# Optimization experiments

Hardware: AMD Instinct MI355X
Metric: run time of the kernel (lower is better)

Reference implementation:

```python
import jax, jax.numpy as jnp
import numpy as np

N_NODES = 200000
IN_DIM = 128
HID = 64
WALK_LEN = 16          # max_step + 1
NUM_WALKS = 16         # = hidden_graphs, walks per graph
N_GRAPHS = 1024
PEN = 32
N_CLASSES = 10
BN_EPS = 1e-5


def setup_inputs() -> dict:
    key = jax.random.key(0)
    ks = jax.random.split(key, 16)
    x = jax.random.normal(ks[0], (N_NODES, IN_DIM), dtype=jnp.float32)
    walks = jax.random.randint(ks[1], (N_GRAPHS * NUM_WALKS, WALK_LEN), 0, N_NODES)
    # each graph contributes NUM_WALKS consecutive walks
    walk_batch = jnp.repeat(jnp.arange(N_GRAPHS), NUM_WALKS)
    s = 1.0 / np.sqrt(HID)
    return {
        "x": x,
        "walks": walks,
        "walk_batch": walk_batch,
        "W_enc": jax.random.normal(ks[2], (HID, IN_DIM), jnp.float32) / np.sqrt(IN_DIM),
        "b_enc": jnp.zeros((HID,), jnp.float32),
        "W_ih": jax.random.uniform(ks[3], (3 * HID, HID), jnp.float32, -s, s),
        "W_hh": jax.random.uniform(ks[4], (3 * HID, HID), jnp.float32, -s, s),
        "b_ih": jax.random.uniform(ks[5], (3 * HID,), jnp.float32, -s, s),
        "b_hh": jax.random.uniform(ks[6], (3 * HID,), jnp.float32, -s, s),
        "gamma": jnp.ones((HID,), jnp.float32),
        "beta": jnp.zeros((HID,), jnp.float32),
        "W1": jax.random.normal(ks[7], (PEN, HID), jnp.float32) / np.sqrt(HID),
        "b1": jnp.zeros((PEN,), jnp.float32),
        "W2": jax.random.normal(ks[8], (N_CLASSES, PEN), jnp.float32) / np.sqrt(PEN),
        "b2": jnp.zeros((N_CLASSES,), jnp.float32),
    }


def _gru_cell(h, xt, W_ih, W_hh, b_ih, b_hh):
    # PyTorch GRU gate math
    gi = xt @ W_ih.T + b_ih            # [W, 3H]
    gh = h @ W_hh.T + b_hh             # [W, 3H]
    i_r, i_z, i_n = jnp.split(gi, 3, axis=-1)
    h_r, h_z, h_n = jnp.split(gh, 3, axis=-1)
    r = jax.nn.sigmoid(i_r + h_r)
    z = jax.nn.sigmoid(i_z + h_z)
    n = jnp.tanh(i_n + r * h_n)
    return (1.0 - z) * n + z * h


def reference(x, walks, walk_batch, W_enc, b_enc, W_ih, W_hh, b_ih, b_hh,
              gamma, beta, W1, b1, W2, b2):
    # feature encoder on all nodes, then gather along walks
    x_enc = x @ W_enc.T + b_enc                     # [N, H]
    walk_feats = x_enc[walks]                       # [W, L, H] gather
    xs = jnp.swapaxes(walk_feats, 0, 1)             # [L, W, H]

    def step(h, xt):
        return _gru_cell(h, xt, W_ih, W_hh, b_ih, b_hh), None

    h0 = jnp.zeros((walks.shape[0], HID), walk_feats.dtype)
    h_final, _ = jax.lax.scan(step, h0, xs)         # [W, H] last hidden state

    # segment-mean pooling per graph
    seg_sum = jax.ops.segment_sum(h_final, walk_batch, num_segments=N_GRAPHS)
    cnt = jax.ops.segment_sum(jnp.ones((walks.shape[0],), h_final.dtype),
                              walk_batch, num_segments=N_GRAPHS)
    graph_enc = seg_sum / jnp.maximum(cnt, 1.0)[:, None]   # [B, H]

    # BatchNorm1d (training mode: batch statistics, biased variance)
    mean = jnp.mean(graph_enc, axis=0)
    var = jnp.mean(jnp.square(graph_enc - mean), axis=0)
    gn = (graph_enc - mean) / jnp.sqrt(var + BN_EPS) * gamma + beta

    h1 = jax.nn.relu(gn @ W1.T + b1)                # dropout p=0 -> identity
    logits = h1 @ W2.T + b2
    return jax.nn.log_softmax(logits, axis=1)
```

## Files before the change

### kernel.cpp

```cpp
#include <hip/hip_runtime.h>
#include <stdint.h>

typedef _Float16 half8 __attribute__((ext_vector_type(8)));
typedef _Float16 half4 __attribute__((ext_vector_type(4)));
typedef float f32x4 __attribute__((ext_vector_type(4)));

#define MFMA_F16(A, B, C) __builtin_amdgcn_mfma_f32_16x16x32_f16(A, B, C, 0, 0, 0)

#define NN 200000
#define NT 3125
#define GSTRIDE 512

__device__ __forceinline__ half8 cvt8(const float* p) {
  half8 a;
#pragma unroll
  for (int e = 0; e < 8; ++e) a[e] = (_Float16)p[e];
  return a;
}

__device__ __forceinline__ void gload_lds16(const void* gp, void* lp) {
  __builtin_amdgcn_global_load_lds(
      (const __attribute__((address_space(1))) uint32_t*)(gp),
      (__attribute__((address_space(3))) uint32_t*)(lp), 16, 0, 0);
}

__global__ __launch_bounds__(256, 2) void k_enc(const float* __restrict__ x,
                                                const float* __restrict__ Wenc,
                                                const float* __restrict__ benc,
                                                _Float16* __restrict__ xenc) {
  __shared__ float xl[2][64 * 128];
  __shared__ _Float16 wlds[16 * 64 * 8];

  const int tid = threadIdx.x;
  const int lane = tid & 63, wv = tid >> 6;
  const int r = lane & 15, g = lane >> 4;

  const int t0 = blockIdx.x;
#pragma unroll
  for (int i = 0; i < 8; ++i) {
    int row = wv * 16 + 2 * i + (lane >> 5);
    int grow = t0 * 64 + row;
    if (grow >= NN) grow = NN - 1;
    int scol = ((lane & 31) * 16) ^ ((row & 7) << 4);
    gload_lds16((const char*)(x + (size_t)grow * 128) + scol,
                (char*)&xl[0][0] + (wv * 16 + 2 * i) * 512);
  }

  for (int i4 = tid; i4 < 2048; i4 += 256) {
    int idx = i4 * 4;
    f32x4 v = *(const f32x4*)(Wenc + idx);
    int j = idx >> 7, k = idx & 127;
    int tile = (j >> 4) * 4 + (k >> 5);
    int ln = ((k >> 3) & 3) * 16 + (j & 15);
    half4 h;
    h[0] = (_Float16)v[0]; h[1] = (_Float16)v[1];
    h[2] = (_Float16)v[2]; h[3] = (_Float16)v[3];
    *(half4*)&wlds[(tile * 64 + ln) * 8 + (k & 7)] = h;
  }
  __syncthreads();

  half8 W[4][4];
#pragma unroll
  for (int jt = 0; jt < 4; ++jt)
#pragma unroll
    for (int kt = 0; kt < 4; ++kt)
      W[jt][kt] = *(const half8*)&wlds[((jt * 4 + kt) * 64 + lane) * 8];

  float bb[4][4];
#pragma unroll
  for (int jt = 0; jt < 4; ++jt)
#pragma unroll
    for (int rr = 0; rr < 4; ++rr) bb[jt][rr] = benc[jt * 16 + g * 4 + rr];

  const int sw = (r & 7) << 4;
  int buf = 0;

  for (int t = t0; t < NT; t += GSTRIDE) {
    int tn = t + GSTRIDE;
    if (tn < NT) {
#pragma unroll
      for (int i = 0; i < 8; ++i) {
        int row = wv * 16 + 2 * i + (lane >> 5);
        int grow = tn * 64 + row;
        if (grow >= NN) grow = NN - 1;
        int scol = ((lane & 31) * 16) ^ ((row & 7) << 4);
        gload_lds16((const char*)(x + (size_t)grow * 128) + scol,
                    (char*)&xl[buf ^ 1][0] + (wv * 16 + 2 * i) * 512);
      }
      asm volatile("s_waitcnt vmcnt(8)" ::: "memory");
    } else {
      asm volatile("s_waitcnt vmcnt(0)" ::: "memory");
    }
    __builtin_amdgcn_sched_barrier(0);

    const char* rp = (const char*)&xl[buf][0] + (wv * 16 + r) * 512;
    f32x4 acc[4];
#pragma unroll
    for (int jt = 0; jt < 4; ++jt)
      acc[jt] = (f32x4){bb[jt][0], bb[jt][1], bb[jt][2], bb[jt][3]};

#pragma unroll
    for (int kt = 0; kt < 4; ++kt) {
      f32x4 v0 = *(const f32x4*)(rp + ((kt * 128 + g * 32) ^ sw));
      f32x4 v1 = *(const f32x4*)(rp + ((kt * 128 + g * 32 + 16) ^ sw));
      half8 a;
#pragma unroll
      for (int e = 0; e < 4; ++e) {
        a[e] = (_Float16)v0[e];
        a[4 + e] = (_Float16)v1[e];
      }
#pragma unroll
      for (int jt = 0; jt < 4; ++jt)
        acc[jt] = MFMA_F16(W[jt][kt], a, acc[jt]);
    }

    int node = t * 64 + wv * 16 + r;
    if (node < NN) {
#pragma unroll
      for (int jt = 0; jt < 4; ++jt) {
        half4 o;
        o[0] = (_Float16)acc[jt][0]; o[1] = (_Float16)acc[jt][1];
        o[2] = (_Float16)acc[jt][2]; o[3] = (_Float16)acc[jt][3];
        *(half4*)&xenc[(size_t)node * 64 + jt * 16 + g * 4] = o;
      }
    }
    buf ^= 1;
  }
}

__global__ __launch_bounds__(256, 1) void k_gru(const _Float16* __restrict__ xenc,
                                                const int* __restrict__ walks,
                                                const float* __restrict__ Wih,
                                                const float* __restrict__ Whh,
                                                const float* __restrict__ bih,
                                                const float* __restrict__ bhh,
                                                float* __restrict__ genc) {
  __shared__ _Float16 wih_lds[24 * 64 * 8];
  __shared__ _Float16 whh_lds[24 * 64 * 8];
  __shared__ _Float16 h_lds[4][16 * 64];
  __shared__ int ids[4][256];

  const int tid = threadIdx.x;
  const int lane = tid & 63, wv = tid >> 6;
  const int r = lane & 15, g = lane >> 4;

  for (int idx = tid; idx < 192 * 64; idx += 256) {
    int j = idx >> 6, k = idx & 63;
    int tile = (j >> 4) * 2 + (k >> 5);
    int ln = ((k >> 3) & 3) * 16 + (j & 15);
    int off = (tile * 64 + ln) * 8 + (k & 7);
    wih_lds[off] = (_Float16)Wih[idx];
    whh_lds[off] = (_Float16)Whh[idx];
  }

  const int gph = blockIdx.x * 4 + wv;
  {
    const int* wp = walks + gph * 256;
    int4 v = *(const int4*)(wp + lane * 4);
    int vals[4] = {v.x, v.y, v.z, v.w};
#pragma unroll
    for (int i = 0; i < 4; ++i) {
      int m = lane * 4 + i;
      ids[wv][(m & 15) * 16 + (m >> 4)] = vals[i];
    }
  }
  for (int i = lane; i < 16 * 64; i += 64) h_lds[wv][i] = (_Float16)0.f;

  __syncthreads();

  half8 Bih[12][2], Bhh[12][2];
#pragma unroll
  for (int jt = 0; jt < 12; ++jt)
#pragma unroll
    for (int kt = 0; kt < 2; ++kt) {
      Bih[jt][kt] = *(const half8*)&wih_lds[((jt * 2 + kt) * 64 + lane) * 8];
      Bhh[jt][kt] = *(const half8*)&whh_lds[((jt * 2 + kt) * 64 + lane) * 8];
    }

  float brz[8], bin4[4], bhn4[4];
#pragma unroll
  for (int jt = 0; jt < 8; ++jt) brz[jt] = bih[jt * 16 + r] + bhh[jt * 16 + r];
#pragma unroll
  for (int jt = 0; jt < 4; ++jt) {
    bin4[jt] = bih[128 + jt * 16 + r];
    bhn4[jt] = bhh[128 + jt * 16 + r];
  }

  f32x4 h[4];
#pragma unroll
  for (int jt = 0; jt < 4; ++jt) h[jt] = (f32x4){0.f, 0.f, 0.f, 0.f};

  char* hbase = (char*)&h_lds[wv][0];
  const int swz = (r & 7) << 4;

  half8 AxA0, AxA1, AxB0, AxB1;
  {
    int n0 = ids[wv][0 * 16 + r];
    const _Float16* p0 = xenc + (size_t)n0 * 64 + g * 8;
    AxA0 = *(const half8*)p0;
    AxA1 = *(const half8*)(p0 + 32);
    int n1 = ids[wv][1 * 16 + r];
    const _Float16* p1 = xenc + (size_t)n1 * 64 + g * 8;
    AxB0 = *(const half8*)p1;
    AxB1 = *(const half8*)(p1 + 32);
  }

#define GRU_STEP(T, AX0, AX1)                                                  \
  {                                                                            \
    half8 Ah0 = *(const half8*)(hbase + ((r * 128 + g * 16) ^ swz));           \
    half8 Ah1 = *(const half8*)(hbase + ((r * 128 + 64 + g * 16) ^ swz));      \
    f32x4 aRZ[8], aIN[4], aHN[4];                                              \
    _Pragma("unroll") for (int jt = 0; jt < 8; ++jt)                           \
        aRZ[jt] = (f32x4){brz[jt], brz[jt], brz[jt], brz[jt]};                 \
    _Pragma("unroll") for (int jt = 0; jt < 4; ++jt) {                         \
      aIN[jt] = (f32x4){bin4[jt], bin4[jt], bin4[jt], bin4[jt]};               \
      aHN[jt] = (f32x4){bhn4[jt], bhn4[jt], bhn4[jt], bhn4[jt]};               \
    }                                                                          \
    _Pragma("unroll") for (int jt = 0; jt < 8; ++jt) {                         \
      aRZ[jt] = MFMA_F16(AX0, Bih[jt][0], aRZ[jt]);                            \
      aRZ[jt] = MFMA_F16(AX1, Bih[jt][1], aRZ[jt]);                            \
    }                                                                          \
    _Pragma("unroll") for (int jt = 0; jt < 4; ++jt) {                         \
      aIN[jt] = MFMA_F16(AX0, Bih[8 + jt][0], aIN[jt]);                        \
      aIN[jt] = MFMA_F16(AX1, Bih[8 + jt][1], aIN[jt]);                        \
    }                                                                          \
                            \
    {                                                                          \
      int nid = ids[wv][(((T) + 2) & 15) * 16 + r];                            \
      const _Float16* xp = xenc + (size_t)nid * 64 + g * 8;                    \
      AX0 = *(const half8*)xp;                                                 \
      AX1 = *(const half8*)(xp + 32);                                          \
    }                                                                          \
    _Pragma("unroll") for (int jt = 0; jt < 8; ++jt) {                         \
      aRZ[jt] = MFMA_F16(Ah0, Bhh[jt][0], aRZ[jt]);                            \
      aRZ[jt] = MFMA_F16(Ah1, Bhh[jt][1], aRZ[jt]);                            \
    }                                                                          \
    _Pragma("unroll") for (int jt = 0; jt < 4; ++jt) {                         \
      aHN[jt] = MFMA_F16(Ah0, Bhh[8 + jt][0], aHN[jt]);                        \
      aHN[jt] = MFMA_F16(Ah1, Bhh[8 + jt][1], aHN[jt]);                        \
    }                                                                          \
    _Pragma("unroll") for (int jt = 0; jt < 4; ++jt)                           \
        _Pragma("unroll") for (int rr = 0; rr < 4; ++rr) {                     \
      float pr = aRZ[jt][rr];                                                  \
      float pz = aRZ[4 + jt][rr];                                              \
      float rg = __builtin_amdgcn_rcpf(1.f + __expf(-pr));                     \
      float zg = __builtin_amdgcn_rcpf(1.f + __expf(-pz));                     \
      float pn = aIN[jt][rr] + rg * aHN[jt][rr];                               \
      float e2 = __expf(2.f * pn);                                             \
      float nn = 1.f - 2.f * __builtin_amdgcn_rcpf(e2 + 1.f);                  \
      h[jt][rr] = (1.f - zg) * nn + zg * h[jt][rr];                            \
    }                                                                          \
    if ((T) < 15) {                                                            \
      _Pragma("unroll") for (int jt = 0; jt < 4; ++jt)                         \
          _Pragma("unroll") for (int rr = 0; rr < 4; ++rr) {                   \
        int row = g * 4 + rr;                                                  \
        int byte = (row * 128 + (jt * 16 + r) * 2) ^ ((row & 7) << 4);         \
        *(_Float16*)(hbase + byte) = (_Float16)h[jt][rr];                      \
      }                                                                        \
    }                                                                          \
  }

  for (int t = 0; t < 16; t += 2) {
    GRU_STEP(t, AxA0, AxA1);
    GRU_STEP(t + 1, AxB0, AxB1);
  }
#undef GRU_STEP

#pragma unroll
  for (int jt = 0; jt < 4; ++jt) {
    float s = h[jt][0] + h[jt][1] + h[jt][2] + h[jt][3];
    s += __shfl_xor(s, 16);
    s += __shfl_xor(s, 32);
    if (g == 0) genc[gph * 64 + jt * 16 + r] = s * 0.0625f;
  }
}

__global__ __launch_bounds__(1024) void k_stats(const float* __restrict__ genc,
                                                const float* __restrict__ gamma,
                                                const float* __restrict__ beta,
                                                float* __restrict__ ss) {
  __shared__ float sum_s[16][64], sq_s[16][64];
  int j = threadIdx.x & 63, grp = threadIdx.x >> 6;
  float s = 0.f, q = 0.f;
#pragma unroll 4
  for (int rr = 0; rr < 64; ++rr) {
    float v = genc[(grp * 64 + rr) * 64 + j];
    s += v;
    q += v * v;
  }
  sum_s[grp][j] = s;
  sq_s[grp][j] = q;
  __syncthreads();
  if (grp == 0) {
    float S = 0.f, Q = 0.f;
#pragma unroll
    for (int k = 0; k < 16; ++k) {
      S += sum_s[k][j];
      Q += sq_s[k][j];
    }
    float mean = S * (1.f / 1024.f);
    float var = Q * (1.f / 1024.f) - mean * mean;
    float rstd = rsqrtf(var + 1e-5f);
    float sc = gamma[j] * rstd;
    ss[j] = sc;
    ss[64 + j] = beta[j] - mean * sc;
  }
}

__global__ __launch_bounds__(256, 1) void k_mlp(const float* __restrict__ genc,
                                                const float* __restrict__ ss,
                                                const float* __restrict__ W1,
                                                const float* __restrict__ b1,
                                                const float* __restrict__ W2,
                                                const float* __restrict__ b2,
                                                float* __restrict__ out) {
  __shared__ float w1[32 * 64], w2[10 * 32], bb1[32], bb2[10], sc[64], sh[64];
  const int tid = threadIdx.x;
  for (int i = tid; i < 32 * 64; i += 256) w1[i] = W1[i];
  for (int i = tid; i < 10 * 32; i += 256) w2[i] = W2[i];
  if (tid < 32) bb1[tid] = b1[tid];
  if (tid >= 32 && tid < 42) bb2[tid - 32] = b2[tid - 32];
  if (tid >= 64 && tid < 128) sc[tid - 64] = ss[tid - 64];
  if (tid >= 128 && tid < 192) sh[tid - 128] = ss[64 + tid - 128];
  __syncthreads();

  const int row = blockIdx.x * 256 + tid;
  float gn[64];
  const f32x4* gp = (const f32x4*)(genc + row * 64);
#pragma unroll
  for (int jq = 0; jq < 16; ++jq) {
    f32x4 v = gp[jq];
#pragma unroll
    for (int e = 0; e < 4; ++e) gn[jq * 4 + e] = v[e] * sc[jq * 4 + e] + sh[jq * 4 + e];
  }

  float h1[32];
#pragma unroll
  for (int i = 0; i < 32; ++i) {
    float a = bb1[i];
#pragma unroll
    for (int j = 0; j < 64; ++j) a += w1[i * 64 + j] * gn[j];
    h1[i] = fmaxf(a, 0.f);
  }

  float lg[10];
  float mx = -1e30f;
#pragma unroll
  for (int c = 0; c < 10; ++c) {
    float a = bb2[c];
#pragma unroll
    for (int i = 0; i < 32; ++i) a += w2[c * 32 + i] * h1[i];
    lg[c] = a;
    mx = fmaxf(mx, a);
  }
  float se = 0.f;
#pragma unroll
  for (int c = 0; c < 10; ++c) se += __expf(lg[c] - mx);
  float lse = mx + __logf(se);
#pragma unroll
  for (int c = 0; c < 10; ++c) out[row * 10 + c] = lg[c] - lse;
}

extern "C" void kernel_launch(void* const* d_in, const int* in_sizes, int n_in,
                              void* d_out, int out_size, void* d_ws, size_t ws_size,
                              hipStream_t stream) {
  const float* x = (const float*)d_in[0];
  const int* walks = (const int*)d_in[1];
  const float* Wenc = (const float*)d_in[3];
  const float* benc = (const float*)d_in[4];
  const float* Wih = (const float*)d_in[5];
  const float* Whh = (const float*)d_in[6];
  const float* bih = (const float*)d_in[7];
  const float* bhh = (const float*)d_in[8];
  const float* gamma = (const float*)d_in[9];
  const float* beta = (const float*)d_in[10];
  const float* W1 = (const float*)d_in[11];
  const float* b1 = (const float*)d_in[12];
  const float* W2 = (const float*)d_in[13];
  const float* b2 = (const float*)d_in[14];
  float* out = (float*)d_out;

  char* ws = (char*)d_ws;
  _Float16* xenc = (_Float16*)ws;
  float* genc = (float*)(ws + 25600000);
  float* ss = (float*)(ws + 25600000 + 262144);

  k_enc<<<dim3(GSTRIDE), dim3(256), 0, stream>>>(x, Wenc, benc, xenc);
  k_gru<<<dim3(256), dim3(256), 0, stream>>>(xenc, walks, Wih, Whh, bih, bhh, genc);
  k_stats<<<dim3(1), dim3(1024), 0, stream>>>(genc, gamma, beta, ss);
  k_mlp<<<dim3(4), dim3(256), 0, stream>>>(genc, ss, W1, b1, W2, b2, out);
}
```

Before: 85.92 us.

## Split each graph's GRU hidden units across two waves with double-buffered h

Each graph's GRU recurrence is now handled by two wavefronts, each computing half of the hidden units, instead of one wave per graph. The grid doubles to 512 blocks with two graphs per block. The hidden state goes through a double-buffered LDS array, and a block-wide barrier after every step exchanges the halves. This halves per-wave MFMA and register work on the serial recurrence and raises occupancy (launch bounds 2), at the cost of 16 barriers per block and duplicated x gathers.

```diff
diff --git a/kernel.cpp b/kernel.cpp
--- a/kernel.cpp
+++ b/kernel.cpp
@@ -128,7 +128,7 @@
   }
 }
 
-__global__ __launch_bounds__(256, 1) void k_gru(const _Float16* __restrict__ xenc,
+__global__ __launch_bounds__(256, 2) void k_gru(const _Float16* __restrict__ xenc,
                                                 const int* __restrict__ walks,
                                                 const float* __restrict__ Wih,
                                                 const float* __restrict__ Whh,
@@ -137,12 +137,15 @@
                                                 float* __restrict__ genc) {
   __shared__ _Float16 wih_lds[24 * 64 * 8];
   __shared__ _Float16 whh_lds[24 * 64 * 8];
-  __shared__ _Float16 h_lds[4][16 * 64];
-  __shared__ int ids[4][256];
+  __shared__ _Float16 h_lds[2][2][16 * 64];
+  __shared__ int ids[2][256];
 
   const int tid = threadIdx.x;
   const int lane = tid & 63, wv = tid >> 6;
   const int r = lane & 15, g = lane >> 4;
+  const int p = wv & 1;
+  const int gl = wv >> 1;
+  const int gph = blockIdx.x * 2 + gl;
 
   for (int idx = tid; idx < 192 * 64; idx += 256) {
     int j = idx >> 6, k = idx & 63;
@@ -153,125 +156,132 @@
     whh_lds[off] = (_Float16)Whh[idx];
   }
 
-  const int gph = blockIdx.x * 4 + wv;
-  {
+  if (p == 0) {
     const int* wp = walks + gph * 256;
     int4 v = *(const int4*)(wp + lane * 4);
     int vals[4] = {v.x, v.y, v.z, v.w};
 #pragma unroll
     for (int i = 0; i < 4; ++i) {
       int m = lane * 4 + i;
-      ids[wv][(m & 15) * 16 + (m >> 4)] = vals[i];
+      ids[gl][(m & 15) * 16 + (m >> 4)] = vals[i];
     }
   }
-  for (int i = lane; i < 16 * 64; i += 64) h_lds[wv][i] = (_Float16)0.f;
+
+  for (int i = tid; i < 2048; i += 256)
+    ((_Float16*)h_lds)[(i >> 10) * 2048 + (i & 1023)] = (_Float16)0.f;
 
   __syncthreads();
 
-  half8 Bih[12][2], Bhh[12][2];
-#pragma unroll
-  for (int jt = 0; jt < 12; ++jt)
-#pragma unroll
-    for (int kt = 0; kt < 2; ++kt) {
-      Bih[jt][kt] = *(const half8*)&wih_lds[((jt * 2 + kt) * 64 + lane) * 8];
-      Bhh[jt][kt] = *(const half8*)&whh_lds[((jt * 2 + kt) * 64 + lane) * 8];
-    }
-
-  float brz[8], bin4[4], bhn4[4];
-#pragma unroll
-  for (int jt = 0; jt < 8; ++jt) brz[jt] = bih[jt * 16 + r] + bhh[jt * 16 + r];
-#pragma unroll
-  for (int jt = 0; jt < 4; ++jt) {
-    bin4[jt] = bih[128 + jt * 16 + r];
-    bhn4[jt] = bhh[128 + jt * 16 + r];
-  }
-
-  f32x4 h[4];
-#pragma unroll
-  for (int jt = 0; jt < 4; ++jt) h[jt] = (f32x4){0.f, 0.f, 0.f, 0.f};
-
-  char* hbase = (char*)&h_lds[wv][0];
+  half8 Bi[3][2][2], Bh[3][2][2];
+#pragma unroll
+  for (int G = 0; G < 3; ++G)
+#pragma unroll
+    for (int jt = 0; jt < 2; ++jt)
+#pragma unroll
+      for (int kt = 0; kt < 2; ++kt) {
+        int T = G * 4 + p * 2 + jt;
+        Bi[G][jt][kt] = *(const half8*)&wih_lds[((T * 2 + kt) * 64 + lane) * 8];
+        Bh[G][jt][kt] = *(const half8*)&whh_lds[((T * 2 + kt) * 64 + lane) * 8];
+      }
+
+  float br[2], bz[2], bin_[2], bhn_[2];
+#pragma unroll
+  for (int jt = 0; jt < 2; ++jt) {
+    int j0 = (p * 2 + jt) * 16 + r;
+    br[jt] = bih[j0] + bhh[j0];
+    bz[jt] = bih[64 + j0] + bhh[64 + j0];
+    bin_[jt] = bih[128 + j0];
+    bhn_[jt] = bhh[128 + j0];
+  }
+
+  f32x4 h[2];
+#pragma unroll
+  for (int jt = 0; jt < 2; ++jt) h[jt] = (f32x4){0.f, 0.f, 0.f, 0.f};
+
   const int swz = (r & 7) << 4;
 
   half8 AxA0, AxA1, AxB0, AxB1;
   {
-    int n0 = ids[wv][0 * 16 + r];
+    int n0 = ids[gl][0 * 16 + r];
     const _Float16* p0 = xenc + (size_t)n0 * 64 + g * 8;
     AxA0 = *(const half8*)p0;
     AxA1 = *(const half8*)(p0 + 32);
-    int n1 = ids[wv][1 * 16 + r];
+    int n1 = ids[gl][1 * 16 + r];
     const _Float16* p1 = xenc + (size_t)n1 * 64 + g * 8;
     AxB0 = *(const half8*)p1;
     AxB1 = *(const half8*)(p1 + 32);
   }
 
-#define GRU_STEP(T, AX0, AX1)                                                  \
+#define GRU_STEP(T, RB, AX0, AX1)                                              \
   {                                                                            \
-    half8 Ah0 = *(const half8*)(hbase + ((r * 128 + g * 16) ^ swz));           \
-    half8 Ah1 = *(const half8*)(hbase + ((r * 128 + 64 + g * 16) ^ swz));      \
-    f32x4 aRZ[8], aIN[4], aHN[4];                                              \
-    _Pragma("unroll") for (int jt = 0; jt < 8; ++jt)                           \
-        aRZ[jt] = (f32x4){brz[jt], brz[jt], brz[jt], brz[jt]};                 \
-    _Pragma("unroll") for (int jt = 0; jt < 4; ++jt) {                         \
-      aIN[jt] = (f32x4){bin4[jt], bin4[jt], bin4[jt], bin4[jt]};               \
-      aHN[jt] = (f32x4){bhn4[jt], bhn4[jt], bhn4[jt], bhn4[jt]};               \
-    }                                                                          \
-    _Pragma("unroll") for (int jt = 0; jt < 8; ++jt) {                         \
-      aRZ[jt] = MFMA_F16(AX0, Bih[jt][0], aRZ[jt]);                            \
-      aRZ[jt] = MFMA_F16(AX1, Bih[jt][1], aRZ[jt]);                            \
-    }                                                                          \
-    _Pragma("unroll") for (int jt = 0; jt < 4; ++jt) {                         \
-      aIN[jt] = MFMA_F16(AX0, Bih[8 + jt][0], aIN[jt]);                        \
-      aIN[jt] = MFMA_F16(AX1, Bih[8 + jt][1], aIN[jt]);                        \
-    }                                                                          \
-                            \
+    char* rbase = (char*)&h_lds[gl][RB][0];                                    \
+    char* wbase = (char*)&h_lds[gl][RB ^ 1][0];                                \
+    half8 Ah0 = *(const half8*)(rbase + ((r * 128 + g * 16) ^ swz));           \
+    half8 Ah1 = *(const half8*)(rbase + ((r * 128 + 64 + g * 16) ^ swz));      \
+    f32x4 aR[2], aZ[2], aN[2], aH[2];                                          \
+    _Pragma("unroll") for (int jt = 0; jt < 2; ++jt) {                         \
+      aR[jt] = (f32x4){br[jt], br[jt], br[jt], br[jt]};                        \
+      aZ[jt] = (f32x4){bz[jt], bz[jt], bz[jt], bz[jt]};                        \
+      aN[jt] = (f32x4){bin_[jt], bin_[jt], bin_[jt], bin_[jt]};                \
+      aH[jt] = (f32x4){bhn_[jt], bhn_[jt], bhn_[jt], bhn_[jt]};                \
+    }                                                                          \
+    _Pragma("unroll") for (int jt = 0; jt < 2; ++jt) {                         \
+      aR[jt] = MFMA_F16(AX0, Bi[0][jt][0], aR[jt]);                            \
+      aR[jt] = MFMA_F16(AX1, Bi[0][jt][1], aR[jt]);                            \
+      aZ[jt] = MFMA_F16(AX0, Bi[1][jt][0], aZ[jt]);                            \
+      aZ[jt] = MFMA_F16(AX1, Bi[1][jt][1], aZ[jt]);                            \
+      aN[jt] = MFMA_F16(AX0, Bi[2][jt][0], aN[jt]);                            \
+      aN[jt] = MFMA_F16(AX1, Bi[2][jt][1], aN[jt]);                            \
+    }                                                                          \
     {                                                                          \
-      int nid = ids[wv][(((T) + 2) & 15) * 16 + r];                            \
+      int nid = ids[gl][(((T) + 2) & 15) * 16 + r];                            \
       const _Float16* xp = xenc + (size_t)nid * 64 + g * 8;                    \
       AX0 = *(const half8*)xp;                                                 \
       AX1 = *(const half8*)(xp + 32);                                          \
     }                                                                          \
-    _Pragma("unroll") for (int jt = 0; jt < 8; ++jt) {                         \
-      aRZ[jt] = MFMA_F16(Ah0, Bhh[jt][0], aRZ[jt]);                            \
-      aRZ[jt] = MFMA_F16(Ah1, Bhh[jt][1], aRZ[jt]);                            \
-    }                                                                          \
-    _Pragma("unroll") for (int jt = 0; jt < 4; ++jt) {                         \
-      aHN[jt] = MFMA_F16(Ah0, Bhh[8 + jt][0], aHN[jt]);                        \
-      aHN[jt] = MFMA_F16(Ah1, Bhh[8 + jt][1], aHN[jt]);                        \
-    }                                                                          \
-    _Pragma("unroll") for (int jt = 0; jt < 4; ++jt)                           \
+    _Pragma("unroll") for (int jt = 0; jt < 2; ++jt) {                         \
+      aR[jt] = MFMA_F16(Ah0, Bh[0][jt][0], aR[jt]);                            \
+      aR[jt] = MFMA_F16(Ah1, Bh[0][jt][1], aR[jt]);                            \
+      aZ[jt] = MFMA_F16(Ah0, Bh[1][jt][0], aZ[jt]);                            \
+      aZ[jt] = MFMA_F16(Ah1, Bh[1][jt][1], aZ[jt]);                            \
+      aH[jt] = MFMA_F16(Ah0, Bh[2][jt][0], aH[jt]);                            \
+      aH[jt] = MFMA_F16(Ah1, Bh[2][jt][1], aH[jt]);                            \
+    }                                                                          \
+    _Pragma("unroll") for (int jt = 0; jt < 2; ++jt)                           \
         _Pragma("unroll") for (int rr = 0; rr < 4; ++rr) {                     \
-      float pr = aRZ[jt][rr];                                                  \
-      float pz = aRZ[4 + jt][rr];                                              \
+      float pr = aR[jt][rr];                                                   \
+      float pz = aZ[jt][rr];                                                   \
       float rg = __builtin_amdgcn_rcpf(1.f + __expf(-pr));                     \
       float zg = __builtin_amdgcn_rcpf(1.f + __expf(-pz));                     \
-      float pn = aIN[jt][rr] + rg * aHN[jt][rr];                               \
+      float pn = aN[jt][rr] + rg * aH[jt][rr];                                 \
       float e2 = __expf(2.f * pn);                                             \
       float nn = 1.f - 2.f * __builtin_amdgcn_rcpf(e2 + 1.f);                  \
-      h[jt][rr] = (1.f - zg) * nn + zg * h[jt][rr];                            \
+      h[jt][rr] = (1.f - zg) * nn + zg * h[jt][rr];                           \
     }                                                                          \
     if ((T) < 15) {                                                            \
-      _Pragma("unroll") for (int jt = 0; jt < 4; ++jt)                         \
+      _Pragma("unroll") for (int jt = 0; jt < 2; ++jt)                         \
           _Pragma("unroll") for (int rr = 0; rr < 4; ++rr) {                   \
         int row = g * 4 + rr;                                                  \
-        int byte = (row * 128 + (jt * 16 + r) * 2) ^ ((row & 7) << 4);         \
-        *(_Float16*)(hbase + byte) = (_Float16)h[jt][rr];                      \
+        int jg = (p * 2 + jt) * 16 + r;                                        \
+        int byte = (row * 128 + jg * 2) ^ ((row & 7) << 4);                    \
+        *(_Float16*)(wbase + byte) = (_Float16)h[jt][rr];                      \
       }                                                                        \
     }                                                                          \
+    __syncthreads();                                                           \
   }
 
   for (int t = 0; t < 16; t += 2) {
-    GRU_STEP(t, AxA0, AxA1);
-    GRU_STEP(t + 1, AxB0, AxB1);
+    GRU_STEP(t, 0, AxA0, AxA1);
+    GRU_STEP(t + 1, 1, AxB0, AxB1);
   }
 #undef GRU_STEP
 
 #pragma unroll
-  for (int jt = 0; jt < 4; ++jt) {
+  for (int jt = 0; jt < 2; ++jt) {
     float s = h[jt][0] + h[jt][1] + h[jt][2] + h[jt][3];
     s += __shfl_xor(s, 16);
     s += __shfl_xor(s, 32);
-    if (g == 0) genc[gph * 64 + jt * 16 + r] = s * 0.0625f;
+    if (g == 0) genc[gph * 64 + (p * 2 + jt) * 16 + r] = s * 0.0625f;
   }
 }
 
@@ -386,7 +396,7 @@
   float* ss = (float*)(ws + 25600000 + 262144);
 
   k_enc<<<dim3(GSTRIDE), dim3(256), 0, stream>>>(x, Wenc, benc, xenc);
-  k_gru<<<dim3(256), dim3(256), 0, stream>>>(xenc, walks, Wih, Whh, bih, bhh, genc);
+  k_gru<<<dim3(512), dim3(256), 0, stream>>>(xenc, walks, Wih, Whh, bih, bhh, genc);
   k_stats<<<dim3(1), dim3(1024), 0, stream>>>(genc, gamma, beta, ss);
   k_mlp<<<dim3(4), dim3(256), 0, stream>>>(genc, ss, W1, b1, W2, b2, out);
 }
```

Measured after the change: 84.04 us. 1.02x faster.
